# Kernel optimization log

Measured on AMD Instinct MI355X. Metric: run time of the kernel, lower is better.

Reference implementation:

```python
import jax, jax.numpy as jnp
import numpy as np

N, DEG, C_IN, C_OUT, T, HID, EPS = 20000, 16, 128, 128, 3, 128, 0.01
MLP_IN = C_IN * (1 + T)


def setup_inputs() -> dict:
    key = jax.random.key(0)
    ks = jax.random.split(key, 14)
    node_attr = jax.random.normal(ks[0], (N, C_IN), jnp.float32)
    # uniform-degree graph: edges sorted by source node (CSR layout)
    src = jnp.repeat(jnp.arange(N, dtype=jnp.int32), DEG)
    dst = jax.random.randint(ks[1], (N * DEG,), 0, N, dtype=jnp.int32)
    edge_index = jnp.stack([src, dst], axis=0)
    slices = jnp.stack([jnp.arange(N, dtype=jnp.int32) * DEG,
                        jnp.full((N,), DEG, jnp.int32)], axis=1)
    s1 = 1.0 / np.sqrt(MLP_IN)
    s2 = 1.0 / np.sqrt(64)
    sg = 1.0 / np.sqrt(HID)
    W1 = jax.random.uniform(ks[2], (MLP_IN, 64), jnp.float32, -s1, s1)
    b1 = jnp.zeros((64,), jnp.float32)
    W2 = jax.random.uniform(ks[3], (64, 1), jnp.float32, -s2, s2)
    b2 = jnp.zeros((1,), jnp.float32)
    Wih = jax.random.uniform(ks[4], (3 * HID, C_IN), jnp.float32, -sg, sg)
    Whh = jax.random.uniform(ks[5], (3 * HID, HID), jnp.float32, -sg, sg)
    bih = jax.random.uniform(ks[6], (3 * HID,), jnp.float32, -sg, sg)
    bhh = jax.random.uniform(ks[7], (3 * HID,), jnp.float32, -sg, sg)
    Wout = jax.random.uniform(ks[8], (HID, C_OUT), jnp.float32, -sg, sg)
    bout = jnp.zeros((C_OUT,), jnp.float32)
    # pre-sampled selection noise (torch.randn per step in the original)
    noise = jax.random.normal(ks[9], (T, N, DEG), jnp.float32)
    return {"node_attr": node_attr, "edge_index": edge_index, "slices": slices,
            "W1": W1, "b1": b1, "W2": W2, "b2": b2,
            "Wih": Wih, "Whh": Whh, "bih": bih, "bhh": bhh,
            "Wout": Wout, "bout": bout, "noise": noise}


def _forward(node_attr, edge_index, W1, b1, W2, b2, Wih, Whh, bih, bhh, Wout, bout, noise):
    v = node_attr
    num_nodes, c = v.shape
    deg = edge_index.shape[1] // num_nodes
    nbr = edge_index[1].reshape(num_nodes, deg)  # uniform-degree CSR neighbors

    walks_last = jnp.arange(num_nodes)
    walk_embeds = jnp.zeros((num_nodes, 1 + T, c), v.dtype).at[:, 0, :].set(v)

    for t in range(T):  # small fixed walk length
        cand = nbr[walks_last]                                   # [N, deg]
        v_t = v[cand]                                            # [N, deg, c]
        we_t = jnp.broadcast_to(walk_embeds[:, None], (num_nodes, deg, 1 + T, c))
        we_t = we_t.at[:, :, 1 + t, :].set(v_t)                  # candidate walk embeds
        flat = we_t.reshape(num_nodes, deg, (1 + T) * c)
        h = jax.nn.relu(flat @ W1 + b1)                          # tiny scoring MLP
        logp = (h @ W2 + b2)[..., 0]                             # [N, deg]
        logp = jax.lax.stop_gradient(logp)                       # torch.no_grad in original
        norm = jax.nn.logsumexp(logp, axis=1, keepdims=True)     # scatter_logsumexp per node
        walk_p = jnp.exp(logp - norm) + EPS * noise[t]
        sel = jnp.argmax(walk_p, axis=1)                         # noisy scatter_max per node
        walks_t = jnp.take_along_axis(cand, sel[:, None], axis=1)[:, 0]
        walk_embeds = walk_embeds.at[:, 1 + t, :].set(v[walks_t])
        walks_last = walks_t

    # GRUAggr: 1-layer GRU (hidden 128) over the walk sequence, then Linear -> C_OUT
    seq = jnp.transpose(walk_embeds, (1, 0, 2))  # [1+T, N, c]

    def gru_step(hprev, x):
        gi = x @ Wih.T + bih
        gh = hprev @ Whh.T + bhh
        ir, iz, inn = jnp.split(gi, 3, axis=-1)
        hr, hz, hn = jnp.split(gh, 3, axis=-1)
        r = jax.nn.sigmoid(ir + hr)
        z = jax.nn.sigmoid(iz + hz)
        n = jnp.tanh(inn + r * hn)
        hnew = (1.0 - z) * n + z * hprev
        return hnew, None

    h0 = jnp.zeros((num_nodes, HID), v.dtype)
    h_last, _ = jax.lax.scan(gru_step, h0, seq)
    return h_last @ Wout + bout  # [N, C_OUT]


def reference(node_attr, edge_index, slices, W1, b1, W2, b2, Wih, Whh, bih, bhh, Wout, bout, noise):
    del slices  # uniform degree encoded directly in edge_index layout
    return _forward(node_attr, edge_index, W1, b1, W2, b2, Wih, Whh, bih, bhh, Wout, bout, noise)
```

## Files before the change

kernel.cpp:

```cpp
#include <hip/hip_runtime.h>
#include <hip/hip_bf16.h>
#include <math.h>

#define NN 20000
#define DEGV 16
#define CINV 128
#define TSTEPS 3
#define HIDV 128

typedef float f32x4 __attribute__((ext_vector_type(4)));
typedef short s16x8 __attribute__((ext_vector_type(8)));

#define MFMA16(a, b, c) __builtin_amdgcn_mfma_f32_16x16x32_bf16(a, b, c, 0, 0, 0)

static __device__ __forceinline__ short f2bf(float x) {
    __hip_bfloat16 h = __float2bfloat16(x);
    return *reinterpret_cast<short*>(&h);
}

__global__ __launch_bounds__(256) void k_precompute(
    const float* __restrict__ v, const float* __restrict__ W1,
    const float* __restrict__ b1,
    float* __restrict__ P, float* __restrict__ base, int* __restrict__ walk_idx,
    short* __restrict__ vb)
{
    __shared__ float vt[32][129];
    int nb = blockIdx.x * 32;
    for (int idx = threadIdx.x; idx < 32 * 128; idx += 256) {
        int nl = idx >> 7, k = idx & 127;
        float x = v[(size_t)(nb + nl) * 128 + k];
        vt[nl][k] = x;
        vb[(size_t)(nb + nl) * 128 + k] = f2bf(x);
    }
    __syncthreads();

    int s  = threadIdx.x >> 6;
    int jg = (threadIdx.x >> 2) & 15;
    int ng = threadIdx.x & 3;

    double accd[8][4];
#pragma unroll
    for (int i = 0; i < 8; ++i)
#pragma unroll
        for (int m = 0; m < 4; ++m) accd[i][m] = 0.0;

    const float* w1s = W1 + (size_t)s * 128 * 64 + jg;

    for (int kb = 0; kb < 8; ++kb) {
        float acc[8][4];
#pragma unroll
        for (int i = 0; i < 8; ++i)
#pragma unroll
            for (int m = 0; m < 4; ++m) acc[i][m] = 0.f;
#pragma unroll
        for (int kk = 0; kk < 16; ++kk) {
            int k = kb * 16 + kk;
            float w0 = w1s[k * 64 +  0];
            float w1 = w1s[k * 64 + 16];
            float w2 = w1s[k * 64 + 32];
            float w3 = w1s[k * 64 + 48];
#pragma unroll
            for (int i = 0; i < 8; ++i) {
                float xv = vt[ng * 8 + i][k];
                acc[i][0] = fmaf(xv, w0, acc[i][0]);
                acc[i][1] = fmaf(xv, w1, acc[i][1]);
                acc[i][2] = fmaf(xv, w2, acc[i][2]);
                acc[i][3] = fmaf(xv, w3, acc[i][3]);
            }
        }
#pragma unroll
        for (int i = 0; i < 8; ++i)
#pragma unroll
            for (int m = 0; m < 4; ++m) accd[i][m] += (double)acc[i][m];
    }

#pragma unroll
    for (int i = 0; i < 8; ++i) {
        int n = nb + ng * 8 + i;
#pragma unroll
        for (int m = 0; m < 4; ++m) {
            int j = jg + 16 * m;
            float pv = (float)accd[i][m];
            P[(size_t)s * NN * 64 + (size_t)n * 64 + j] = pv;
            if (s == 0) {
                base[(size_t)n * 64 + j] = pv + b1[j];
                if (j == 0) walk_idx[n] = n;
            }
        }
    }
}

__global__ __launch_bounds__(256) void k_walk_step(
    const float* __restrict__ P, float* __restrict__ base,
    const int* __restrict__ dst, const float* __restrict__ W2,
    const float* __restrict__ b2, const float* __restrict__ noise,
    int* __restrict__ walk_idx, int t)
{
    int wave = threadIdx.x >> 6;
    int lane = threadIdx.x & 63;
    int n = blockIdx.x * 4 + wave;
    if (n >= NN) return;

    int wl = walk_idx[t * NN + n];
    int d = lane >> 2, sub = lane & 3;
    int cand = dst[wl * DEGV + d];

    const float* Pslice = P + (size_t)(t + 1) * NN * 64;
    const float4* b4 = (const float4*)(base + (size_t)n * 64);
    const float4* p4 = (const float4*)(Pslice + (size_t)cand * 64);
    const float4* w4 = (const float4*)W2;

    double acc = 0.0;
#pragma unroll
    for (int k = 0; k < 4; ++k) {
        float4 bb = b4[sub * 4 + k];
        float4 pp = p4[sub * 4 + k];
        float4 ww = w4[sub * 4 + k];
        acc += (double)fmaxf(bb.x + pp.x, 0.f) * (double)ww.x;
        acc += (double)fmaxf(bb.y + pp.y, 0.f) * (double)ww.y;
        acc += (double)fmaxf(bb.z + pp.z, 0.f) * (double)ww.z;
        acc += (double)fmaxf(bb.w + pp.w, 0.f) * (double)ww.w;
    }
    acc += __shfl_xor(acc, 1);
    acc += __shfl_xor(acc, 2);
    double logp = acc + (double)b2[0];

    double m = logp;
    for (int mask = 4; mask < 64; mask <<= 1) m = fmax(m, __shfl_xor(m, mask));
    double e = exp(logp - m);
    double ssum = e;
    for (int mask = 4; mask < 64; mask <<= 1) ssum += __shfl_xor(ssum, mask);
    double norm = m + log(ssum);

    double wp = exp(logp - norm) +
                0.01 * (double)noise[((size_t)t * NN + n) * DEGV + d];

    int bd = d;
    double bwp = wp;
    for (int mask = 4; mask < 64; mask <<= 1) {
        double owp = __shfl_xor(bwp, mask);
        int od = __shfl_xor(bd, mask);
        if (owp > bwp || (owp == bwp && od < bd)) { bwp = owp; bd = od; }
    }
    int sel = dst[wl * DEGV + bd];

    base[(size_t)n * 64 + lane] += Pslice[(size_t)sel * 64 + lane];
    if (lane == 0) walk_idx[(t + 1) * NN + n] = sel;
}

__global__ __launch_bounds__(256) void k_convert_w(
    const float* __restrict__ Wih, const float* __restrict__ Whh,
    const float* __restrict__ Wout,
    short* __restrict__ Wihb, short* __restrict__ Whhb, short* __restrict__ WoutTb)
{
    int idx = blockIdx.x * 256 + threadIdx.x;
    if (idx < 49152) {
        Wihb[idx] = f2bf(Wih[idx]);
    } else if (idx < 98304) {
        int e = idx - 49152;
        Whhb[e] = f2bf(Whh[e]);
    } else if (idx < 114688) {
        int e = idx - 98304;
        int o = e >> 7, k = e & 127;
        WoutTb[e] = f2bf(Wout[k * 128 + o]);
    }
}

__global__ __launch_bounds__(512, 4) void k_gru_fused(
    const short* __restrict__ vb, const int* __restrict__ widx,
    const short* __restrict__ Wihb, const short* __restrict__ Whhb,
    const short* __restrict__ WoutTb,
    const float* __restrict__ bih, const float* __restrict__ bhh,
    const float* __restrict__ bout, float* __restrict__ out)
{
    __shared__ short x_bf[32][136];
    __shared__ short h_bf[32][136];
    int tid = threadIdx.x;
    int j = tid >> 6, lane = tid & 63;
    int c = lane & 15, q = lane >> 4;
    int nb = blockIdx.x * 32;
    int u = j * 16 + c;

    float b_r  = bih[u] + bhh[u];
    float b_z  = bih[128 + u] + bhh[128 + u];
    float b_in = bih[256 + u];
    float b_hn = bhh[256 + u];

    float h_reg[2][4];
#pragma unroll
    for (int g = 0; g < 2; ++g)
#pragma unroll
        for (int i = 0; i < 4; ++i) h_reg[g][i] = 0.f;

    const short* bi_base = Wihb + c * 128 + q * 8 + j * 2048;
    const short* bh_base = Whhb + c * 128 + q * 8 + j * 2048;

#pragma unroll 1
    for (int t = 0; t < 1 + TSTEPS; ++t) {
        {
            int row = tid >> 4, chunk = tid & 15;
            int src = widx[t * NN + nb + row];
            *(s16x8*)&x_bf[row][chunk * 8] =
                *(const s16x8*)(vb + (size_t)src * 128 + chunk * 8);
        }
        __syncthreads();

        float rr[2][4], zz[2][4];

        {
            f32x4 zf = {0.f, 0.f, 0.f, 0.f};
            f32x4 aR[2] = {zf, zf}, aZ[2] = {zf, zf};
#pragma unroll
            for (int ks = 0; ks < 4; ++ks) {
                s16x8 biR = *(const s16x8*)(bi_base + ks * 32);
                s16x8 biZ = *(const s16x8*)(bi_base + 8 * 2048 + ks * 32);
#pragma unroll
                for (int g = 0; g < 2; ++g) {
                    s16x8 a = *(const s16x8*)&x_bf[g * 16 + c][ks * 32 + q * 8];
                    aR[g] = MFMA16(a, biR, aR[g]);
                    aZ[g] = MFMA16(a, biZ, aZ[g]);
                }
            }
            if (t > 0) {
#pragma unroll
                for (int ks = 0; ks < 4; ++ks) {
                    s16x8 bhR = *(const s16x8*)(bh_base + ks * 32);
                    s16x8 bhZ = *(const s16x8*)(bh_base + 8 * 2048 + ks * 32);
#pragma unroll
                    for (int g = 0; g < 2; ++g) {
                        s16x8 a = *(const s16x8*)&h_bf[g * 16 + c][ks * 32 + q * 8];
                        aR[g] = MFMA16(a, bhR, aR[g]);
                        aZ[g] = MFMA16(a, bhZ, aZ[g]);
                    }
                }
            }
#pragma unroll
            for (int g = 0; g < 2; ++g)
#pragma unroll
                for (int i = 0; i < 4; ++i) {
                    rr[g][i] = 1.f / (1.f + __expf(-(aR[g][i] + b_r)));
                    zz[g][i] = 1.f / (1.f + __expf(-(aZ[g][i] + b_z)));
                }
        }

        {
            f32x4 zf = {0.f, 0.f, 0.f, 0.f};
            f32x4 aIN[2] = {zf, zf}, aHN[2] = {zf, zf};
#pragma unroll
            for (int ks = 0; ks < 4; ++ks) {
                s16x8 biN = *(const s16x8*)(bi_base + 16 * 2048 + ks * 32);
#pragma unroll
                for (int g = 0; g < 2; ++g) {
                    s16x8 a = *(const s16x8*)&x_bf[g * 16 + c][ks * 32 + q * 8];
                    aIN[g] = MFMA16(a, biN, aIN[g]);
                }
            }
            if (t > 0) {
#pragma unroll
                for (int ks = 0; ks < 4; ++ks) {
                    s16x8 bhN = *(const s16x8*)(bh_base + 16 * 2048 + ks * 32);
#pragma unroll
                    for (int g = 0; g < 2; ++g) {
                        s16x8 a = *(const s16x8*)&h_bf[g * 16 + c][ks * 32 + q * 8];
                        aHN[g] = MFMA16(a, bhN, aHN[g]);
                    }
                }
            }
            __syncthreads();
#pragma unroll
            for (int g = 0; g < 2; ++g)
#pragma unroll
                for (int i = 0; i < 4; ++i) {
                    float narg = aIN[g][i] + b_in + rr[g][i] * (aHN[g][i] + b_hn);
                    float e2 = __expf(2.f * narg);
                    float ngt = 1.f - 2.f / (e2 + 1.f);
                    float hn = (1.f - zz[g][i]) * ngt + zz[g][i] * h_reg[g][i];
                    h_reg[g][i] = hn;
                    h_bf[g * 16 + q * 4 + i][u] = f2bf(hn);
                }
        }
        __syncthreads();
    }

    {
        const short* bo_base = WoutTb + c * 128 + q * 8 + j * 2048;
        f32x4 zf = {0.f, 0.f, 0.f, 0.f};
        f32x4 acco[2] = {zf, zf};
#pragma unroll
        for (int ks = 0; ks < 4; ++ks) {
            s16x8 bo = *(const s16x8*)(bo_base + ks * 32);
#pragma unroll
            for (int g = 0; g < 2; ++g) {
                s16x8 a = *(const s16x8*)&h_bf[g * 16 + c][ks * 32 + q * 8];
                acco[g] = MFMA16(a, bo, acco[g]);
            }
        }
        float bb = bout[u];
#pragma unroll
        for (int g = 0; g < 2; ++g)
#pragma unroll
            for (int i = 0; i < 4; ++i)
                out[(size_t)(nb + g * 16 + q * 4 + i) * 128 + u] = acco[g][i] + bb;
    }
}

extern "C" void kernel_launch(void* const* d_in, const int* in_sizes, int n_in,
                              void* d_out, int out_size, void* d_ws, size_t ws_size,
                              hipStream_t stream)
{
    const float* node_attr = (const float*)d_in[0];
    const int*   edge_index = (const int*)d_in[1];
    const float* W1  = (const float*)d_in[3];
    const float* b1  = (const float*)d_in[4];
    const float* W2  = (const float*)d_in[5];
    const float* b2  = (const float*)d_in[6];
    const float* Wih = (const float*)d_in[7];
    const float* Whh = (const float*)d_in[8];
    const float* bih = (const float*)d_in[9];
    const float* bhh = (const float*)d_in[10];
    const float* Wout = (const float*)d_in[11];
    const float* bout = (const float*)d_in[12];
    const float* noise = (const float*)d_in[13];

    const int* dst = edge_index + (size_t)NN * DEGV;

    char* ws = (char*)d_ws;
    size_t offP    = 0;
    size_t offBase = offP + (size_t)4 * NN * 64 * 4;
    size_t offW    = offBase + (size_t)NN * 64 * 4;
    size_t offWidx = offW + (size_t)(2 * 49152 + 16384) * 2;
    size_t offVb   = offWidx + (size_t)4 * NN * 4;
    float* P    = (float*)(ws + offP);
    float* base = (float*)(ws + offBase);
    short* Wihb   = (short*)(ws + offW);
    short* Whhb   = Wihb + 384 * 128;
    short* WoutTb = Whhb + 384 * 128;
    int*   widx = (int*)(ws + offWidx);
    short* vb   = (short*)(ws + offVb);

    dim3 blk(256);
    k_convert_w<<<dim3(448), blk, 0, stream>>>(Wih, Whh, Wout, Wihb, Whhb, WoutTb);
    k_precompute<<<dim3(625), blk, 0, stream>>>(node_attr, W1, b1, P, base, widx, vb);
    for (int t = 0; t < TSTEPS; ++t)
        k_walk_step<<<dim3(5000), blk, 0, stream>>>(P, base, dst, W2, b2, noise, widx, t);
    k_gru_fused<<<dim3(625), dim3(512), 0, stream>>>(vb, widx, Wihb, Whhb, WoutTb,
                                                     bih, bhh, bout, (float*)d_out);
}
```

Measured before the change: 166.3 us.

## Keep GRU weights in registers and double-buffer the next walk-step gather

Loads all Wih, Whh and Wout bf16 fragments into registers once before the time loop instead of reloading them from global memory each step. It also prefetches the next step's gathered node embeddings into registers while the current step's MFMAs run, writing them into a second LDS buffer after the barrier. This removes one barrier per step and hides gather latency. In exchange it raises register pressure, so launch bounds drop from 4 to 2 blocks per CU, which lowers occupancy.

```diff
diff --git a/kernel.cpp b/kernel.cpp
--- a/kernel.cpp
+++ b/kernel.cpp
@@ -166,14 +166,14 @@
     }
 }
 
-__global__ __launch_bounds__(512, 4) void k_gru_fused(
+__global__ __launch_bounds__(512, 2) void k_gru_fused(
     const short* __restrict__ vb, const int* __restrict__ widx,
     const short* __restrict__ Wihb, const short* __restrict__ Whhb,
     const short* __restrict__ WoutTb,
     const float* __restrict__ bih, const float* __restrict__ bhh,
     const float* __restrict__ bout, float* __restrict__ out)
 {
-    __shared__ short x_bf[32][136];
+    __shared__ short x_bf[2][32][136];
     __shared__ short h_bf[32][136];
     int tid = threadIdx.x;
     int j = tid >> 6, lane = tid & 63;
@@ -186,24 +186,46 @@
     float b_in = bih[256 + u];
     float b_hn = bhh[256 + u];
 
+    const short* bi_base = Wihb   + c * 128 + q * 8 + j * 2048;
+    const short* bh_base = Whhb   + c * 128 + q * 8 + j * 2048;
+    const short* bo_base = WoutTb + c * 128 + q * 8 + j * 2048;
+
+    s16x8 wiR[4], wiZ[4], wiN[4], whR[4], whZ[4], whN[4], wo[4];
+#pragma unroll
+    for (int ks = 0; ks < 4; ++ks) {
+        wiR[ks] = *(const s16x8*)(bi_base + ks * 32);
+        wiZ[ks] = *(const s16x8*)(bi_base + 8 * 2048 + ks * 32);
+        wiN[ks] = *(const s16x8*)(bi_base + 16 * 2048 + ks * 32);
+        whR[ks] = *(const s16x8*)(bh_base + ks * 32);
+        whZ[ks] = *(const s16x8*)(bh_base + 8 * 2048 + ks * 32);
+        whN[ks] = *(const s16x8*)(bh_base + 16 * 2048 + ks * 32);
+        wo[ks]  = *(const s16x8*)(bo_base + ks * 32);
+    }
+
     float h_reg[2][4];
 #pragma unroll
     for (int g = 0; g < 2; ++g)
 #pragma unroll
         for (int i = 0; i < 4; ++i) h_reg[g][i] = 0.f;
 
-    const short* bi_base = Wihb + c * 128 + q * 8 + j * 2048;
-    const short* bh_base = Whhb + c * 128 + q * 8 + j * 2048;
+    int srow = tid >> 4, schunk = tid & 15;
+
+    {
+        int src = widx[nb + srow];
+        *(s16x8*)&x_bf[0][srow][schunk * 8] =
+            *(const s16x8*)(vb + (size_t)src * 128 + schunk * 8);
+    }
+    __syncthreads();
 
 #pragma unroll 1
     for (int t = 0; t < 1 + TSTEPS; ++t) {
-        {
-            int row = tid >> 4, chunk = tid & 15;
-            int src = widx[t * NN + nb + row];
-            *(s16x8*)&x_bf[row][chunk * 8] =
-                *(const s16x8*)(vb + (size_t)src * 128 + chunk * 8);
-        }
-        __syncthreads();
+        int cur = t & 1;
+
+        s16x8 pref;
+        if (t < TSTEPS) {
+            int src = widx[(t + 1) * NN + nb + srow];
+            pref = *(const s16x8*)(vb + (size_t)src * 128 + schunk * 8);
+        }
 
         float rr[2][4], zz[2][4];
 
@@ -212,25 +234,21 @@
             f32x4 aR[2] = {zf, zf}, aZ[2] = {zf, zf};
 #pragma unroll
             for (int ks = 0; ks < 4; ++ks) {
-                s16x8 biR = *(const s16x8*)(bi_base + ks * 32);
-                s16x8 biZ = *(const s16x8*)(bi_base + 8 * 2048 + ks * 32);
 #pragma unroll
                 for (int g = 0; g < 2; ++g) {
-                    s16x8 a = *(const s16x8*)&x_bf[g * 16 + c][ks * 32 + q * 8];
-                    aR[g] = MFMA16(a, biR, aR[g]);
-                    aZ[g] = MFMA16(a, biZ, aZ[g]);
+                    s16x8 a = *(const s16x8*)&x_bf[cur][g * 16 + c][ks * 32 + q * 8];
+                    aR[g] = MFMA16(a, wiR[ks], aR[g]);
+                    aZ[g] = MFMA16(a, wiZ[ks], aZ[g]);
                 }
             }
             if (t > 0) {
 #pragma unroll
                 for (int ks = 0; ks < 4; ++ks) {
-                    s16x8 bhR = *(const s16x8*)(bh_base + ks * 32);
-                    s16x8 bhZ = *(const s16x8*)(bh_base + 8 * 2048 + ks * 32);
 #pragma unroll
                     for (int g = 0; g < 2; ++g) {
                         s16x8 a = *(const s16x8*)&h_bf[g * 16 + c][ks * 32 + q * 8];
-                        aR[g] = MFMA16(a, bhR, aR[g]);
-                        aZ[g] = MFMA16(a, bhZ, aZ[g]);
+                        aR[g] = MFMA16(a, whR[ks], aR[g]);
+                        aZ[g] = MFMA16(a, whZ[ks], aZ[g]);
                     }
                 }
             }
@@ -248,25 +266,25 @@
             f32x4 aIN[2] = {zf, zf}, aHN[2] = {zf, zf};
 #pragma unroll
             for (int ks = 0; ks < 4; ++ks) {
-                s16x8 biN = *(const s16x8*)(bi_base + 16 * 2048 + ks * 32);
 #pragma unroll
                 for (int g = 0; g < 2; ++g) {
-                    s16x8 a = *(const s16x8*)&x_bf[g * 16 + c][ks * 32 + q * 8];
-                    aIN[g] = MFMA16(a, biN, aIN[g]);
+                    s16x8 a = *(const s16x8*)&x_bf[cur][g * 16 + c][ks * 32 + q * 8];
+                    aIN[g] = MFMA16(a, wiN[ks], aIN[g]);
                 }
             }
             if (t > 0) {
 #pragma unroll
                 for (int ks = 0; ks < 4; ++ks) {
-                    s16x8 bhN = *(const s16x8*)(bh_base + 16 * 2048 + ks * 32);
 #pragma unroll
                     for (int g = 0; g < 2; ++g) {
                         s16x8 a = *(const s16x8*)&h_bf[g * 16 + c][ks * 32 + q * 8];
-                        aHN[g] = MFMA16(a, bhN, aHN[g]);
+                        aHN[g] = MFMA16(a, whN[ks], aHN[g]);
                     }
                 }
             }
             __syncthreads();
+            if (t < TSTEPS)
+                *(s16x8*)&x_bf[cur ^ 1][srow][schunk * 8] = pref;
 #pragma unroll
             for (int g = 0; g < 2; ++g)
 #pragma unroll
@@ -283,16 +301,14 @@
     }
 
     {
-        const short* bo_base = WoutTb + c * 128 + q * 8 + j * 2048;
         f32x4 zf = {0.f, 0.f, 0.f, 0.f};
         f32x4 acco[2] = {zf, zf};
 #pragma unroll
         for (int ks = 0; ks < 4; ++ks) {
-            s16x8 bo = *(const s16x8*)(bo_base + ks * 32);
 #pragma unroll
             for (int g = 0; g < 2; ++g) {
                 s16x8 a = *(const s16x8*)&h_bf[g * 16 + c][ks * 32 + q * 8];
-                acco[g] = MFMA16(a, bo, acco[g]);
+                acco[g] = MFMA16(a, wo[ks], acco[g]);
             }
         }
         float bb = bout[u];
```

New measurement: 168.5 us. About the same (+1.4%).

## Fuse walk steps into one kernel, swizzle LDS, use custom double exp

Applied to the files above, without the earlier changes.

Merges the three per-step walk kernel launches into a single kernel that keeps each node's base accumulator and W2 slice in registers across steps. This removes two launches and the global read-modify-write of base between steps. It also replaces the library double exp and log with a polynomial exp and a direct division for the softmax. Separately, the precompute kernel gets an XOR-swizzled, float4-vectorized LDS layout to cut bank conflicts and LDS instruction count. The custom exp trades a small amount of accuracy, which could flip near-tie argmax selections.

```diff
diff --git a/kernel.cpp b/kernel.cpp
--- a/kernel.cpp
+++ b/kernel.cpp
@@ -18,18 +18,43 @@
     return *reinterpret_cast<short*>(&h);
 }
 
+static __device__ __forceinline__ double exp_fast(double x) {
+    const double LOG2E = 1.4426950408889634074;
+    const double LN2HI = 6.93147180369123816490e-01;
+    const double LN2LO = 1.90821492927058770002e-10;
+    double fn = floor(fma(x, LOG2E, 0.5));
+    double r  = fma(fn, -LN2HI, x);
+    r = fma(fn, -LN2LO, r);
+    double p = 2.08767569878680989792e-09;
+    p = fma(p, r, 2.50521083854417187751e-08);
+    p = fma(p, r, 2.75573192239858906526e-07);
+    p = fma(p, r, 2.75573192239858925110e-06);
+    p = fma(p, r, 2.48015873015873015873e-05);
+    p = fma(p, r, 1.98412698412698412526e-04);
+    p = fma(p, r, 1.38888888888888894568e-03);
+    p = fma(p, r, 8.33333333333333321769e-03);
+    p = fma(p, r, 4.16666666666666643537e-02);
+    p = fma(p, r, 1.66666666666666657415e-01);
+    p = fma(p, r, 5.0e-01);
+    p = fma(p, r, 1.0);
+    p = fma(p, r, 1.0);
+    long long bits = __double_as_longlong(p) + ((long long)(int)fn << 52);
+    return __longlong_as_double(bits);
+}
+
 __global__ __launch_bounds__(256) void k_precompute(
     const float* __restrict__ v, const float* __restrict__ W1,
     const float* __restrict__ b1,
     float* __restrict__ P, float* __restrict__ base, int* __restrict__ walk_idx,
     short* __restrict__ vb)
 {
-    __shared__ float vt[32][129];
+    __shared__ float vt[32][132];
     int nb = blockIdx.x * 32;
     for (int idx = threadIdx.x; idx < 32 * 128; idx += 256) {
         int nl = idx >> 7, k = idx & 127;
         float x = v[(size_t)(nb + nl) * 128 + k];
-        vt[nl][k] = x;
+        int k4 = (k >> 2) ^ (nl >> 3);
+        vt[nl][(k4 << 2) | (k & 3)] = x;
         vb[(size_t)(nb + nl) * 128 + k] = f2bf(x);
     }
     __syncthreads();
@@ -53,19 +78,28 @@
 #pragma unroll
             for (int m = 0; m < 4; ++m) acc[i][m] = 0.f;
 #pragma unroll
-        for (int kk = 0; kk < 16; ++kk) {
-            int k = kb * 16 + kk;
-            float w0 = w1s[k * 64 +  0];
-            float w1 = w1s[k * 64 + 16];
-            float w2 = w1s[k * 64 + 32];
-            float w3 = w1s[k * 64 + 48];
-#pragma unroll
-            for (int i = 0; i < 8; ++i) {
-                float xv = vt[ng * 8 + i][k];
-                acc[i][0] = fmaf(xv, w0, acc[i][0]);
-                acc[i][1] = fmaf(xv, w1, acc[i][1]);
-                acc[i][2] = fmaf(xv, w2, acc[i][2]);
-                acc[i][3] = fmaf(xv, w3, acc[i][3]);
+        for (int kq = 0; kq < 4; ++kq) {
+            int K4 = kb * 4 + kq;
+            float4 xv[8];
+#pragma unroll
+            for (int i = 0; i < 8; ++i)
+                xv[i] = *(const float4*)&vt[ng * 8 + i][(K4 ^ ng) << 2];
+#pragma unroll
+            for (int kk = 0; kk < 4; ++kk) {
+                int k = K4 * 4 + kk;
+                float w0 = w1s[k * 64 +  0];
+                float w1 = w1s[k * 64 + 16];
+                float w2 = w1s[k * 64 + 32];
+                float w3 = w1s[k * 64 + 48];
+#pragma unroll
+                for (int i = 0; i < 8; ++i) {
+                    float x = (kk == 0) ? xv[i].x : (kk == 1) ? xv[i].y
+                            : (kk == 2) ? xv[i].z : xv[i].w;
+                    acc[i][0] = fmaf(x, w0, acc[i][0]);
+                    acc[i][1] = fmaf(x, w1, acc[i][1]);
+                    acc[i][2] = fmaf(x, w2, acc[i][2]);
+                    acc[i][3] = fmaf(x, w3, acc[i][3]);
+                }
             }
         }
 #pragma unroll
@@ -90,62 +124,76 @@
     }
 }
 
-__global__ __launch_bounds__(256) void k_walk_step(
-    const float* __restrict__ P, float* __restrict__ base,
+__global__ __launch_bounds__(256) void k_walk_fused(
+    const float* __restrict__ P, const float* __restrict__ base_g,
     const int* __restrict__ dst, const float* __restrict__ W2,
     const float* __restrict__ b2, const float* __restrict__ noise,
-    int* __restrict__ walk_idx, int t)
+    int* __restrict__ walk_idx)
 {
     int wave = threadIdx.x >> 6;
     int lane = threadIdx.x & 63;
     int n = blockIdx.x * 4 + wave;
-    if (n >= NN) return;
-
-    int wl = walk_idx[t * NN + n];
     int d = lane >> 2, sub = lane & 3;
-    int cand = dst[wl * DEGV + d];
-
-    const float* Pslice = P + (size_t)(t + 1) * NN * 64;
-    const float4* b4 = (const float4*)(base + (size_t)n * 64);
-    const float4* p4 = (const float4*)(Pslice + (size_t)cand * 64);
-    const float4* w4 = (const float4*)W2;
-
-    double acc = 0.0;
-#pragma unroll
-    for (int k = 0; k < 4; ++k) {
-        float4 bb = b4[sub * 4 + k];
-        float4 pp = p4[sub * 4 + k];
-        float4 ww = w4[sub * 4 + k];
-        acc += (double)fmaxf(bb.x + pp.x, 0.f) * (double)ww.x;
-        acc += (double)fmaxf(bb.y + pp.y, 0.f) * (double)ww.y;
-        acc += (double)fmaxf(bb.z + pp.z, 0.f) * (double)ww.z;
-        acc += (double)fmaxf(bb.w + pp.w, 0.f) * (double)ww.w;
-    }
-    acc += __shfl_xor(acc, 1);
-    acc += __shfl_xor(acc, 2);
-    double logp = acc + (double)b2[0];
-
-    double m = logp;
-    for (int mask = 4; mask < 64; mask <<= 1) m = fmax(m, __shfl_xor(m, mask));
-    double e = exp(logp - m);
-    double ssum = e;
-    for (int mask = 4; mask < 64; mask <<= 1) ssum += __shfl_xor(ssum, mask);
-    double norm = m + log(ssum);
-
-    double wp = exp(logp - norm) +
-                0.01 * (double)noise[((size_t)t * NN + n) * DEGV + d];
-
-    int bd = d;
-    double bwp = wp;
-    for (int mask = 4; mask < 64; mask <<= 1) {
-        double owp = __shfl_xor(bwp, mask);
-        int od = __shfl_xor(bd, mask);
-        if (owp > bwp || (owp == bwp && od < bd)) { bwp = owp; bd = od; }
-    }
-    int sel = dst[wl * DEGV + bd];
-
-    base[(size_t)n * 64 + lane] += Pslice[(size_t)sel * 64 + lane];
-    if (lane == 0) walk_idx[(t + 1) * NN + n] = sel;
+
+    float4 base_r[4], w2r[4];
+    {
+        const float4* bg = (const float4*)(base_g + (size_t)n * 64 + sub * 16);
+        const float4* wg = ((const float4*)W2) + sub * 4;
+#pragma unroll
+        for (int k = 0; k < 4; ++k) { base_r[k] = bg[k]; w2r[k] = wg[k]; }
+    }
+    double b2d = (double)b2[0];
+
+    int wl = n;
+#pragma unroll 1
+    for (int t = 0; t < TSTEPS; ++t) {
+        const float* Pslice = P + (size_t)(t + 1) * NN * 64;
+        int cand = dst[wl * DEGV + d];
+        const float4* p4 = (const float4*)(Pslice + (size_t)cand * 64 + sub * 16);
+
+        double acc = 0.0;
+#pragma unroll
+        for (int k = 0; k < 4; ++k) {
+            float4 bb = base_r[k];
+            float4 pp = p4[k];
+            float4 ww = w2r[k];
+            acc += (double)fmaxf(bb.x + pp.x, 0.f) * (double)ww.x;
+            acc += (double)fmaxf(bb.y + pp.y, 0.f) * (double)ww.y;
+            acc += (double)fmaxf(bb.z + pp.z, 0.f) * (double)ww.z;
+            acc += (double)fmaxf(bb.w + pp.w, 0.f) * (double)ww.w;
+        }
+        acc += __shfl_xor(acc, 1);
+        acc += __shfl_xor(acc, 2);
+        double logp = acc + b2d;
+
+        double m = logp;
+        for (int mask = 4; mask < 64; mask <<= 1) m = fmax(m, __shfl_xor(m, mask));
+        double e = exp_fast(logp - m);
+        double ssum = e;
+        for (int mask = 4; mask < 64; mask <<= 1) ssum += __shfl_xor(ssum, mask);
+
+        double wp = e / ssum +
+                    0.01 * (double)noise[((size_t)t * NN + n) * DEGV + d];
+
+        int bd = d;
+        double bwp = wp;
+        for (int mask = 4; mask < 64; mask <<= 1) {
+            double owp = __shfl_xor(bwp, mask);
+            int od = __shfl_xor(bd, mask);
+            if (owp > bwp || (owp == bwp && od < bd)) { bwp = owp; bd = od; }
+        }
+        int sel = dst[wl * DEGV + bd];
+
+        const float4* ps = (const float4*)(Pslice + (size_t)sel * 64 + sub * 16);
+#pragma unroll
+        for (int k = 0; k < 4; ++k) {
+            float4 pv = ps[k];
+            base_r[k].x += pv.x; base_r[k].y += pv.y;
+            base_r[k].z += pv.z; base_r[k].w += pv.w;
+        }
+        if (lane == 0) walk_idx[(t + 1) * NN + n] = sel;
+        wl = sel;
+    }
 }
 
 __global__ __launch_bounds__(256) void k_convert_w(
@@ -341,8 +389,7 @@
     dim3 blk(256);
     k_convert_w<<<dim3(448), blk, 0, stream>>>(Wih, Whh, Wout, Wihb, Whhb, WoutTb);
     k_precompute<<<dim3(625), blk, 0, stream>>>(node_attr, W1, b1, P, base, widx, vb);
-    for (int t = 0; t < TSTEPS; ++t)
-        k_walk_step<<<dim3(5000), blk, 0, stream>>>(P, base, dst, W2, b2, noise, widx, t);
+    k_walk_fused<<<dim3(5000), blk, 0, stream>>>(P, base, dst, W2, b2, noise, widx);
     k_gru_fused<<<dim3(625), dim3(512), 0, stream>>>(vb, widx, Wihb, Whhb, WoutTb,
                                                      bih, bhh, bout, (float*)d_out);
 }
```

Measured after the change: 156.2 us. 1.06x faster.
